# Performance work log

Hardware: AMD Instinct MI355X
Metric: run time of the kernel (lower is better)

Reference implementation:

```python
import jax, jax.numpy as jnp
import numpy as np

H = 512   # GRU hidden
I = 12    # feature dim
Z = 64    # latent dim


def setup_inputs() -> dict:
    key = jax.random.key(0)
    ks = jax.random.split(key, 24)
    B, T = 256, 256
    rn = lambda k, shape, s: (jax.random.normal(k, shape, dtype=jnp.float32) * s)
    sg = 1.0 / np.sqrt(H)
    inp = {
        'x': rn(ks[0], (B, T, I), 1.0),
        'eps': rn(ks[1], (B, Z), 1.0),
        # encoder GRU (torch layout: gates stacked r,z,n)
        'w_ih_e': rn(ks[2], (3 * H, I), sg), 'w_hh_e': rn(ks[3], (3 * H, H), sg),
        'b_ih_e': rn(ks[4], (3 * H,), sg), 'b_hh_e': rn(ks[5], (3 * H,), sg),
        # decoder GRU
        'w_ih_d': rn(ks[6], (3 * H, I), sg), 'w_hh_d': rn(ks[7], (3 * H, H), sg),
        'b_ih_d': rn(ks[8], (3 * H,), sg), 'b_hh_d': rn(ks[9], (3 * H,), sg),
        # linear heads (torch nn.Linear layout: [out, in])
        'fc1_w': rn(ks[10], (256, H), 1 / np.sqrt(H)), 'fc1_b': rn(ks[11], (256,), 0.02),
        'fc11_w': rn(ks[12], (Z, 256), 1 / np.sqrt(256)), 'fc11_b': rn(ks[13], (Z,), 0.02),
        'fc12_w': rn(ks[14], (Z, 256), 1 / np.sqrt(256)), 'fc12_b': rn(ks[15], (Z,), 0.02),
        'fc2_w': rn(ks[16], (256, Z), 1 / np.sqrt(Z)), 'fc2_b': rn(ks[17], (256,), 0.02),
        'fc3_w': rn(ks[18], (H, 256), 1 / np.sqrt(256)), 'fc3_b': rn(ks[19], (H,), 0.02),
        'fc4_w': rn(ks[20], (I, H), 1 / np.sqrt(H)), 'fc4_b': rn(ks[21], (I,), 0.02),
    }
    return inp


def gru_step(x, h, w_ih, w_hh, b_ih, b_hh):
    # torch GRU cell: gates ordered (r, z, n)
    gi = x @ w_ih.T + b_ih            # [B, 3H]
    gh = h @ w_hh.T + b_hh            # [B, 3H]
    i_r, i_z, i_n = jnp.split(gi, 3, axis=-1)
    h_r, h_z, h_n = jnp.split(gh, 3, axis=-1)
    r = jax.nn.sigmoid(i_r + h_r)
    z = jax.nn.sigmoid(i_z + h_z)
    n = jnp.tanh(i_n + r * h_n)
    return (1.0 - z) * n + z * h


def reference(x, eps, w_ih_e, w_hh_e, b_ih_e, b_hh_e, w_ih_d, w_hh_d, b_ih_d, b_hh_d,
              fc1_w, fc1_b, fc11_w, fc11_b, fc12_w, fc12_b, fc2_w, fc2_b,
              fc3_w, fc3_b, fc4_w, fc4_b):
    B, T, _ = x.shape
    lrelu = lambda v: jax.nn.leaky_relu(v, 0.01)

    # ---- encoder GRU over time ----
    h0 = jnp.zeros((B, H), x.dtype)
    def enc(h, xt):
        return gru_step(xt, h, w_ih_e, w_hh_e, b_ih_e, b_hh_e), None
    h_enc, _ = jax.lax.scan(enc, h0, jnp.swapaxes(x, 0, 1))  # final hidden [B,H]

    # ---- latent head ----
    v = lrelu(h_enc)
    v = lrelu(v @ fc1_w.T + fc1_b)
    mu = v @ fc11_w.T + fc11_b
    log_var = v @ fc12_w.T + fc12_b
    std = jnp.exp(0.5 * log_var)
    z_lat = mu + std * eps            # reparameterized rsample

    # ---- decoder init ----
    u = lrelu(z_lat @ fc2_w.T + fc2_b)
    h_dec = u @ fc3_w.T + fc3_b       # [B,H]

    y0 = jnp.zeros((B, I), x.dtype)
    def dec(carry, _):
        y, h = carry
        h = gru_step(y, h, w_ih_d, w_hh_d, b_ih_d, b_hh_d)
        y = h @ fc4_w.T + fc4_b
        return (y, h), y
    _, seq = jax.lax.scan(dec, (y0, h_dec), None, length=T)  # [T,B,I]
    seq = jnp.swapaxes(seq, 0, 1)     # [B,T,I]
    return seq, mu, log_var
```

## Files before the change

kernel.cpp:

```cpp
#include <hip/hip_runtime.h>
#include <hip/hip_bf16.h>

#define DI 12
#define DH 512
#define DT 256
#define DB 256
#define SCOPE __HIP_MEMORY_SCOPE_AGENT

typedef float f32x4 __attribute__((ext_vector_type(4)));
typedef __bf16 bf16x8 __attribute__((ext_vector_type(8)));

__device__ __forceinline__ float sigm(float x) { return 1.f / (1.f + __expf(-x)); }
__device__ __forceinline__ float tanh_f(float x) {
    float xc = fminf(fmaxf(x, -15.f), 15.f);
    float e = __expf(-2.f * xc);
    return (1.f - e) / (1.f + e);
}
__device__ __forceinline__ float lrelu(float x) { return x > 0.f ? x : 0.01f * x; }
__device__ __forceinline__ unsigned short f2bf(float f) {
    return __builtin_bit_cast(unsigned short, (__bf16)f);
}

__device__ __forceinline__ void stage_h(unsigned short* hbuf, const unsigned long long* src2, int tid) {
    unsigned long long tmp[11];
    #pragma unroll
    for (int j = 0; j < 11; ++j) {
        int i = tid + j * 384;
        if (i < 4096) tmp[j] = __hip_atomic_load(src2 + i, __ATOMIC_RELAXED, SCOPE);
    }
    #pragma unroll
    for (int j = 0; j < 11; ++j) {
        int i = tid + j * 384;
        if (i < 4096) {
            int row = i >> 7, dq = i & 127;
            unsigned off = (unsigned)row * 1024u + (((unsigned)(dq * 8)) ^ ((unsigned)((row & 7) << 4)));
            *(unsigned long long*)((char*)hbuf + off) = tmp[j];
        }
    }
}

__device__ __forceinline__ void barrier_wait(const unsigned* fl, int wave, int lane, unsigned gen) {
    if (wave == 0) {
        while (true) {
            unsigned v = __hip_atomic_load(fl + (lane & 31), __ATOMIC_RELAXED, SCOPE);
            if (__all((int)(v >= gen))) break;
            __builtin_amdgcn_s_sleep(1);
        }
        __builtin_amdgcn_fence(__ATOMIC_ACQUIRE, "agent");
    }
}

__device__ __forceinline__ f32x4 mfma_hbuf(const unsigned short* hbuf, const bf16x8* bw,
                                           int arow, int lk) {
    f32x4 acc = {0.f, 0.f, 0.f, 0.f};
    const unsigned rbase = (unsigned)arow * 1024u;
    const unsigned swz = (unsigned)((arow & 7) << 4);
    const char* hb = (const char*)hbuf;
    #pragma unroll
    for (int kk = 0; kk < 16; ++kk) {
        unsigned off = rbase + (((unsigned)(kk * 64 + lk * 16)) ^ swz);
        bf16x8 a = *(const bf16x8*)(hb + off);
        acc = __builtin_amdgcn_mfma_f32_16x16x32_bf16(a, bw[kk], acc, 0, 0, 0);
    }
    return acc;
}

__global__ void init_kernel(unsigned* flE, unsigned* flD) {
    if (blockIdx.x == 0) flE[threadIdx.x] = 0u;
    else flD[threadIdx.x] = 0u;
}

__global__ void prep_kernel(const float* __restrict__ w_ih_d, const float* __restrict__ fc4_w,
                            const float* __restrict__ b_ih_d, const float* __restrict__ fc4_b,
                            unsigned short* __restrict__ W2bf, float* __restrict__ b2,
                            unsigned short* __restrict__ fc4bf)
{
    const int r = blockIdx.x, tid = threadIdx.x;
    if (r < 3 * DH) {
        float wr[DI];
        #pragma unroll
        for (int k = 0; k < DI; ++k) wr[k] = w_ih_d[r * DI + k];
        int c0 = tid * 4;
        #pragma unroll
        for (int q = 0; q < 4; ++q) {
            int c = c0 + q;
            float a = 0.f;
            #pragma unroll
            for (int k = 0; k < DI; ++k) a += wr[k] * fc4_w[k * DH + c];
            W2bf[(size_t)r * DH + c] = f2bf(a);
        }
        if (tid == 0) {
            float a = b_ih_d[r];
            #pragma unroll
            for (int k = 0; k < DI; ++k) a += wr[k] * fc4_b[k];
            b2[r] = a;
        }
    } else {
        int rr = r - 3 * DH;
        int c0 = tid * 4;
        #pragma unroll
        for (int q = 0; q < 4; ++q)
            fc4bf[rr * DH + c0 + q] = (rr < DI) ? f2bf(fc4_w[rr * DH + c0 + q]) : (unsigned short)0;
    }
}

__global__ __launch_bounds__(384, 2)
void enc_kernel(const float* __restrict__ x, const float* __restrict__ w_ih,
                const float* __restrict__ w_hh, const float* __restrict__ b_ih,
                const float* __restrict__ b_hh, unsigned* __restrict__ hpp,
                float* __restrict__ hencF, unsigned* __restrict__ flags)
{
    const int tid = threadIdx.x;
    const int bid = blockIdx.x;
    const int bg = bid & 7;
    const int cb = bid >> 3;
    const int growbase = bg * 32;
    const int ub = cb * 16;
    const int wave = tid >> 6, lane = tid & 63;
    const int rt = wave / 3, g = wave % 3;
    const int lrow = lane & 15, lk = lane >> 4;
    unsigned* flg = flags + bg * 32;

    __shared__ unsigned short hbuf[32 * DH];
    __shared__ float xbuf[32][DI];
    __shared__ float RZ[2][2][16][16];

    const int grow = g * DH + ub + lrow;
    const float bhh_l = b_hh[grow];
    const float bih_l = b_ih[grow];
    float wihr[DI];
    #pragma unroll
    for (int k = 0; k < DI; ++k) wihr[k] = w_ih[grow * DI + k];

    for (int i = tid; i < 32 * DH / 2; i += 384) ((unsigned*)hbuf)[i] = 0u;
    {
        int r = tid / DI, c = tid % DI;
        xbuf[r][c] = x[(size_t)(growbase + r) * (DT * DI) + c];
    }

    bf16x8 bfr[16];
    {
        const float* wr = w_hh + (size_t)grow * DH;
        #pragma unroll
        for (int kk = 0; kk < 16; ++kk) {
            const float* p = wr + kk * 32 + lk * 8;
            bf16x8 v;
            #pragma unroll
            for (int j = 0; j < 8; ++j) v[j] = (__bf16)p[j];
            bfr[kk] = v;
        }
    }
    float hreg[4] = {0.f, 0.f, 0.f, 0.f};
    const int pid = (g != 2) ? ((rt * 2 + g) * 64 + lane) : 0;
    __syncthreads();

    for (int t = 0; t < DT; ++t) {
        const bool lastt = (t == DT - 1);
        f32x4 acc = mfma_hbuf(hbuf, bfr, rt * 16 + lrow, lk);
        float gi[4];
        #pragma unroll
        for (int i = 0; i < 4; ++i) {
            int row = rt * 16 + lk * 4 + i;
            float a2 = bih_l;
            #pragma unroll
            for (int k = 0; k < DI; ++k) a2 += xbuf[row][k] * wihr[k];
            gi[i] = a2;
        }
        float hn[4], gin[4];
        if (g == 0) {
            #pragma unroll
            for (int i = 0; i < 4; ++i)
                RZ[0][rt][lk * 4 + i][lrow] = sigm(acc[i] + bhh_l + gi[i]);
        } else if (g == 1) {
            #pragma unroll
            for (int i = 0; i < 4; ++i)
                RZ[1][rt][lk * 4 + i][lrow] = sigm(acc[i] + bhh_l + gi[i]);
        } else {
            #pragma unroll
            for (int i = 0; i < 4; ++i) { hn[i] = acc[i] + bhh_l; gin[i] = gi[i]; }
        }
        float xr0 = 0.f, xr1 = 0.f;
        if (g != 2 && !lastt) {
            xr0 = x[(size_t)(growbase + pid / 12) * (DT * DI) + (size_t)(t + 1) * DI + pid % 12];
            if (pid < 128) {
                int e = 256 + pid;
                xr1 = x[(size_t)(growbase + e / 12) * (DT * DI) + (size_t)(t + 1) * DI + e % 12];
            }
        }
        __syncthreads();
        if (g == 2) {
            unsigned* dst = hpp + ((t + 1) & 1) * (DB * DH / 2);
            #pragma unroll
            for (int i = 0; i < 4; ++i) {
                int ri = lk * 4 + i;
                int row = rt * 16 + ri;
                float r = RZ[0][rt][ri][lrow];
                float z = RZ[1][rt][ri][lrow];
                float n = tanh_f(gin[i] + r * hn[i]);
                hreg[i] = (1.f - z) * n + z * hreg[i];
                float hp = __shfl_xor(hreg[i], 1);
                if (!lastt) {
                    if (!(lrow & 1)) {
                        unsigned val = (unsigned)f2bf(hreg[i]) | ((unsigned)f2bf(hp) << 16);
                        __hip_atomic_store(dst + (unsigned)(growbase + row) * 256u +
                                           (unsigned)(cb * 8 + (lrow >> 1)),
                                           val, __ATOMIC_RELAXED, SCOPE);
                    }
                } else {
                    hencF[(size_t)(growbase + row) * DH + ub + lrow] = hreg[i];
                }
            }
        }
        if (lastt) break;
        __syncthreads();
        const unsigned gen = (unsigned)(t + 1);
        if (tid == 0) __hip_atomic_store(flg + cb, gen, __ATOMIC_RELAXED, SCOPE);
        barrier_wait(flg, wave, lane, gen);
        __syncthreads();
        stage_h(hbuf, (const unsigned long long*)(hpp + ((t + 1) & 1) * (DB * DH / 2)) +
                      (size_t)growbase * 128, tid);
        if (g != 2) {
            xbuf[pid / 12][pid % 12] = xr0;
            if (pid < 128) { int e = 256 + pid; xbuf[e / 12][e % 12] = xr1; }
        }
        __syncthreads();
    }
}

__global__ void mid_kernel(const float* __restrict__ henc, const float* __restrict__ eps,
                           const float* __restrict__ fc1_w, const float* __restrict__ fc1_b,
                           const float* __restrict__ fc11_w, const float* __restrict__ fc11_b,
                           const float* __restrict__ fc12_w, const float* __restrict__ fc12_b,
                           const float* __restrict__ fc2_w, const float* __restrict__ fc2_b,
                           const float* __restrict__ fc3_w, const float* __restrict__ fc3_b,
                           float* __restrict__ hdecF, unsigned* __restrict__ hppD0,
                           float* __restrict__ out)
{
    const int row = blockIdx.x, tid = threadIdx.x;
    __shared__ float v0[512], v1[256], zb[64], ubuf[256];
    for (int k = tid; k < 512; k += 256) v0[k] = lrelu(henc[(size_t)row * 512 + k]);
    __syncthreads();
    {
        float a = fc1_b[tid];
        const float* w = fc1_w + (size_t)tid * 512;
        for (int k = 0; k < 512; k += 4) {
            float4 wv = *(const float4*)(w + k);
            a += wv.x * v0[k] + wv.y * v0[k + 1] + wv.z * v0[k + 2] + wv.w * v0[k + 3];
        }
        v1[tid] = lrelu(a);
    }
    __syncthreads();
    if (tid < 64) {
        float m = fc11_b[tid], lv = fc12_b[tid];
        const float* w1 = fc11_w + (size_t)tid * 256;
        const float* w2 = fc12_w + (size_t)tid * 256;
        for (int k = 0; k < 256; k += 4) {
            float4 a = *(const float4*)(w1 + k);
            float4 b = *(const float4*)(w2 + k);
            m  += a.x * v1[k] + a.y * v1[k + 1] + a.z * v1[k + 2] + a.w * v1[k + 3];
            lv += b.x * v1[k] + b.y * v1[k + 1] + b.z * v1[k + 2] + b.w * v1[k + 3];
        }
        out[786432 + row * 64 + tid] = m;
        out[802816 + row * 64 + tid] = lv;
        zb[tid] = m + __expf(0.5f * lv) * eps[row * 64 + tid];
    }
    __syncthreads();
    {
        float a = fc2_b[tid];
        const float* w = fc2_w + (size_t)tid * 64;
        for (int k = 0; k < 64; k += 4) {
            float4 wv = *(const float4*)(w + k);
            a += wv.x * zb[k] + wv.y * zb[k + 1] + wv.z * zb[k + 2] + wv.w * zb[k + 3];
        }
        ubuf[tid] = lrelu(a);
    }
    __syncthreads();
    {
        float hv[2];
        #pragma unroll
        for (int q = 0; q < 2; ++q) {
            int j = 2 * tid + q;
            float a = fc3_b[j];
            const float* w = fc3_w + (size_t)j * 256;
            for (int k = 0; k < 256; k += 4) {
                float4 wv = *(const float4*)(w + k);
                a += wv.x * ubuf[k] + wv.y * ubuf[k + 1] + wv.z * ubuf[k + 2] + wv.w * ubuf[k + 3];
            }
            hdecF[(size_t)row * 512 + j] = a;
            hv[q] = a;
        }
        hppD0[row * 256 + tid] = (unsigned)f2bf(hv[0]) | ((unsigned)f2bf(hv[1]) << 16);
    }
}

__global__ __launch_bounds__(384, 2)
void dec_kernel(const float* __restrict__ w_hh, const float* __restrict__ b_ih,
                const float* __restrict__ b_hh, const unsigned short* __restrict__ W2bf,
                const float* __restrict__ b2, const unsigned short* __restrict__ fc4bf,
                const float* __restrict__ fc4_b, const float* __restrict__ hdecF,
                unsigned* __restrict__ hpp, unsigned* __restrict__ flags,
                float* __restrict__ out)
{
    const int tid = threadIdx.x;
    const int bid = blockIdx.x;
    const int bg = bid & 7;
    const int cb = bid >> 3;
    const int growbase = bg * 32;
    const int ub = cb * 16;
    const int wave = tid >> 6, lane = tid & 63;
    const int rt = wave / 3, g = wave % 3;
    const int lrow = lane & 15, lk = lane >> 4;
    unsigned* flg = flags + bg * 32;

    __shared__ unsigned short hbuf[32 * DH];
    __shared__ float RZ[2][2][16][16];

    const int grow = g * DH + ub + lrow;
    const float bhh_l = b_hh[grow];
    const float bih_l = b_ih[grow];
    const float b2_l  = b2[grow];
    const float fb4_l = (lrow < DI) ? fc4_b[lrow] : 0.f;

    bf16x8 bfr[16];
    {
        const float* wr = w_hh + (size_t)grow * DH;
        #pragma unroll
        for (int kk = 0; kk < 16; ++kk) {
            const float* p = wr + kk * 32 + lk * 8;
            bf16x8 v;
            #pragma unroll
            for (int j = 0; j < 8; ++j) v[j] = (__bf16)p[j];
            bfr[kk] = v;
        }
    }
    bf16x8 w2fr[16];
    {
        const unsigned short* wr = W2bf + (size_t)grow * DH;
        #pragma unroll
        for (int kk = 0; kk < 16; ++kk)
            w2fr[kk] = *reinterpret_cast<const bf16x8*>(wr + kk * 32 + lk * 8);
    }
    float hreg[4] = {0.f, 0.f, 0.f, 0.f};
    if (g == 2) {
        #pragma unroll
        for (int i = 0; i < 4; ++i)
            hreg[i] = hdecF[(size_t)(growbase + rt * 16 + lk * 4 + i) * DH + ub + lrow];
    }
    stage_h(hbuf, (const unsigned long long*)hpp + (size_t)growbase * 128, tid);
    __syncthreads();

    const bool ywave = (g == 0) && (cb == 0);
    const unsigned short* fp = fc4bf + (size_t)lrow * DH;

    for (int t = 0; t < DT; ++t) {
        f32x4 acc1 = {0.f, 0.f, 0.f, 0.f};
        f32x4 acc2 = {0.f, 0.f, 0.f, 0.f};
        {
            const int arow = rt * 16 + lrow;
            const unsigned rbase = (unsigned)arow * 1024u;
            const unsigned swz = (unsigned)((arow & 7) << 4);
            const char* hb = (const char*)hbuf;
            if (t == 0) {
                #pragma unroll
                for (int kk = 0; kk < 16; ++kk) {
                    unsigned off = rbase + (((unsigned)(kk * 64 + lk * 16)) ^ swz);
                    bf16x8 a = *(const bf16x8*)(hb + off);
                    acc1 = __builtin_amdgcn_mfma_f32_16x16x32_bf16(a, bfr[kk], acc1, 0, 0, 0);
                }
            } else {
                #pragma unroll
                for (int kk = 0; kk < 16; ++kk) {
                    unsigned off = rbase + (((unsigned)(kk * 64 + lk * 16)) ^ swz);
                    bf16x8 a = *(const bf16x8*)(hb + off);
                    acc1 = __builtin_amdgcn_mfma_f32_16x16x32_bf16(a, bfr[kk], acc1, 0, 0, 0);
                    acc2 = __builtin_amdgcn_mfma_f32_16x16x32_bf16(a, w2fr[kk], acc2, 0, 0, 0);
                }
            }
        }
        if (ywave && t > 0) {
            f32x4 ya = {0.f, 0.f, 0.f, 0.f};
            const int arow = rt * 16 + lrow;
            const unsigned rbase = (unsigned)arow * 1024u;
            const unsigned swz = (unsigned)((arow & 7) << 4);
            const char* hb = (const char*)hbuf;
            #pragma unroll
            for (int kk = 0; kk < 16; ++kk) {
                unsigned off = rbase + (((unsigned)(kk * 64 + lk * 16)) ^ swz);
                bf16x8 a = *(const bf16x8*)(hb + off);
                bf16x8 yb = *reinterpret_cast<const bf16x8*>(fp + kk * 32 + lk * 8);
                ya = __builtin_amdgcn_mfma_f32_16x16x32_bf16(a, yb, ya, 0, 0, 0);
            }
            if (lrow < DI) {
                #pragma unroll
                for (int i = 0; i < 4; ++i)
                    out[(size_t)(growbase + rt * 16 + lk * 4 + i) * (DT * DI) +
                        (size_t)(t - 1) * DI + lrow] = ya[i] + fb4_l;
            }
        }
        const float bsel = (t == 0) ? bih_l : b2_l;
        float hn[4], gin[4];
        if (g == 0) {
            #pragma unroll
            for (int i = 0; i < 4; ++i)
                RZ[0][rt][lk * 4 + i][lrow] = sigm(acc1[i] + bhh_l + acc2[i] + bsel);
        } else if (g == 1) {
            #pragma unroll
            for (int i = 0; i < 4; ++i)
                RZ[1][rt][lk * 4 + i][lrow] = sigm(acc1[i] + bhh_l + acc2[i] + bsel);
        } else {
            #pragma unroll
            for (int i = 0; i < 4; ++i) { hn[i] = acc1[i] + bhh_l; gin[i] = acc2[i] + bsel; }
        }
        __syncthreads();
        if (g == 2) {
            unsigned* dst = hpp + ((t + 1) & 1) * (DB * DH / 2);
            #pragma unroll
            for (int i = 0; i < 4; ++i) {
                int ri = lk * 4 + i;
                int row = rt * 16 + ri;
                float r = RZ[0][rt][ri][lrow];
                float z = RZ[1][rt][ri][lrow];
                float n = tanh_f(gin[i] + r * hn[i]);
                hreg[i] = (1.f - z) * n + z * hreg[i];
                float hp = __shfl_xor(hreg[i], 1);
                if (!(lrow & 1)) {
                    unsigned val = (unsigned)f2bf(hreg[i]) | ((unsigned)f2bf(hp) << 16);
                    __hip_atomic_store(dst + (unsigned)(growbase + row) * 256u +
                                       (unsigned)(cb * 8 + (lrow >> 1)),
                                       val, __ATOMIC_RELAXED, SCOPE);
                }
            }
        }
        __syncthreads();
        const unsigned gen = (unsigned)(t + 1);
        if (tid == 0) __hip_atomic_store(flg + cb, gen, __ATOMIC_RELAXED, SCOPE);
        barrier_wait(flg, wave, lane, gen);
        __syncthreads();
        stage_h(hbuf, (const unsigned long long*)(hpp + ((t + 1) & 1) * (DB * DH / 2)) +
                      (size_t)growbase * 128, tid);
        __syncthreads();
    }
    if (ywave) {
        f32x4 ya = {0.f, 0.f, 0.f, 0.f};
        const int arow = rt * 16 + lrow;
        const unsigned rbase = (unsigned)arow * 1024u;
        const unsigned swz = (unsigned)((arow & 7) << 4);
        const char* hb = (const char*)hbuf;
        #pragma unroll
        for (int kk = 0; kk < 16; ++kk) {
            unsigned off = rbase + (((unsigned)(kk * 64 + lk * 16)) ^ swz);
            bf16x8 a = *(const bf16x8*)(hb + off);
            bf16x8 yb = *reinterpret_cast<const bf16x8*>(fp + kk * 32 + lk * 8);
            ya = __builtin_amdgcn_mfma_f32_16x16x32_bf16(a, yb, ya, 0, 0, 0);
        }
        if (lrow < DI) {
            #pragma unroll
            for (int i = 0; i < 4; ++i)
                out[(size_t)(growbase + rt * 16 + lk * 4 + i) * (DT * DI) +
                    (size_t)(DT - 1) * DI + lrow] = ya[i] + fb4_l;
        }
    }
}

extern "C" void kernel_launch(void* const* d_in, const int* in_sizes, int n_in,
                              void* d_out, int out_size, void* d_ws, size_t ws_size,
                              hipStream_t stream)
{
    const float* x      = (const float*)d_in[0];
    const float* eps    = (const float*)d_in[1];
    const float* w_ih_e = (const float*)d_in[2];
    const float* w_hh_e = (const float*)d_in[3];
    const float* b_ih_e = (const float*)d_in[4];
    const float* b_hh_e = (const float*)d_in[5];
    const float* w_ih_d = (const float*)d_in[6];
    const float* w_hh_d = (const float*)d_in[7];
    const float* b_ih_d = (const float*)d_in[8];
    const float* b_hh_d = (const float*)d_in[9];
    const float* fc1_w  = (const float*)d_in[10];
    const float* fc1_b  = (const float*)d_in[11];
    const float* fc11_w = (const float*)d_in[12];
    const float* fc11_b = (const float*)d_in[13];
    const float* fc12_w = (const float*)d_in[14];
    const float* fc12_b = (const float*)d_in[15];
    const float* fc2_w  = (const float*)d_in[16];
    const float* fc2_b  = (const float*)d_in[17];
    const float* fc3_w  = (const float*)d_in[18];
    const float* fc3_b  = (const float*)d_in[19];
    const float* fc4_w  = (const float*)d_in[20];
    const float* fc4_b  = (const float*)d_in[21];

    char* ws = (char*)d_ws;
    unsigned* hppE        = (unsigned*)(ws + 0);
    unsigned* hppD        = (unsigned*)(ws + 524288);
    float* hencF          = (float*)(ws + 1048576);
    float* hdecF          = (float*)(ws + 1572864);
    unsigned* flagE       = (unsigned*)(ws + 2097152);
    unsigned* flagD       = (unsigned*)(ws + 2101248);
    unsigned short* W2bf  = (unsigned short*)(ws + 2105344);
    float* b2             = (float*)(ws + 3678208);
    unsigned short* fc4bf = (unsigned short*)(ws + 3684352);
    float* out = (float*)d_out;

    init_kernel<<<2, 256, 0, stream>>>(flagE, flagD);
    prep_kernel<<<1552, 128, 0, stream>>>(w_ih_d, fc4_w, b_ih_d, fc4_b, W2bf, b2, fc4bf);
    enc_kernel<<<256, 384, 0, stream>>>(x, w_ih_e, w_hh_e, b_ih_e, b_hh_e, hppE, hencF, flagE);
    mid_kernel<<<256, 256, 0, stream>>>(hencF, eps, fc1_w, fc1_b, fc11_w, fc11_b,
                                        fc12_w, fc12_b, fc2_w, fc2_b, fc3_w, fc3_b,
                                        hdecF, hppD, out);
    dec_kernel<<<256, 384, 0, stream>>>(w_hh_d, b_ih_d, b_hh_d, W2bf, b2, fc4bf, fc4_b,
                                        hdecF, hppD, flagD, out);
}
```

Measured before the change: 3.306 ms.

## Signal per-wave release flags and drop pre-barrier block sync in GRU steps

Each h-producing wave now publishes its own release-ordered flag (64 flags per batch group) as soon as its stores are done, replacing the block-wide __syncthreads plus single-thread relaxed flag store. Polling moves to wave 1, which waits on all 64 flags. In the decoder, the fc4 output MFMA is moved into the else branch so it runs alongside the flag publish and no longer precedes the gate computation. This removes one block barrier per timestep and shortens the critical path between computing h and signalling it. The cost is more flag traffic and a larger polling footprint.

```diff
diff --git a/kernel.cpp b/kernel.cpp
--- a/kernel.cpp
+++ b/kernel.cpp
@@ -39,15 +39,13 @@
     }
 }
 
-__device__ __forceinline__ void barrier_wait(const unsigned* fl, int wave, int lane, unsigned gen) {
-    if (wave == 0) {
-        while (true) {
-            unsigned v = __hip_atomic_load(fl + (lane & 31), __ATOMIC_RELAXED, SCOPE);
-            if (__all((int)(v >= gen))) break;
-            __builtin_amdgcn_s_sleep(1);
-        }
-        __builtin_amdgcn_fence(__ATOMIC_ACQUIRE, "agent");
-    }
+__device__ __forceinline__ void poll64(const unsigned* fl, int lane, unsigned gen) {
+    while (true) {
+        unsigned v = __hip_atomic_load(fl + lane, __ATOMIC_RELAXED, SCOPE);
+        if (__all((int)(v >= gen))) break;
+        __builtin_amdgcn_s_sleep(1);
+    }
+    __builtin_amdgcn_fence(__ATOMIC_ACQUIRE, "agent");
 }
 
 __device__ __forceinline__ f32x4 mfma_hbuf(const unsigned short* hbuf, const bf16x8* bw,
@@ -66,8 +64,9 @@
 }
 
 __global__ void init_kernel(unsigned* flE, unsigned* flD) {
-    if (blockIdx.x == 0) flE[threadIdx.x] = 0u;
-    else flD[threadIdx.x] = 0u;
+    int i = blockIdx.x * 256 + threadIdx.x;
+    if (i < 512) flE[i] = 0u;
+    else flD[i - 512] = 0u;
 }
 
 __global__ void prep_kernel(const float* __restrict__ w_ih_d, const float* __restrict__ fc4_w,
@@ -119,7 +118,7 @@
     const int wave = tid >> 6, lane = tid & 63;
     const int rt = wave / 3, g = wave % 3;
     const int lrow = lane & 15, lk = lane >> 4;
-    unsigned* flg = flags + bg * 32;
+    unsigned* flg = flags + bg * 64;
 
     __shared__ unsigned short hbuf[32 * DH];
     __shared__ float xbuf[32][DI];
@@ -189,33 +188,41 @@
         }
         __syncthreads();
         if (g == 2) {
-            unsigned* dst = hpp + ((t + 1) & 1) * (DB * DH / 2);
-            #pragma unroll
-            for (int i = 0; i < 4; ++i) {
-                int ri = lk * 4 + i;
-                int row = rt * 16 + ri;
-                float r = RZ[0][rt][ri][lrow];
-                float z = RZ[1][rt][ri][lrow];
-                float n = tanh_f(gin[i] + r * hn[i]);
-                hreg[i] = (1.f - z) * n + z * hreg[i];
-                float hp = __shfl_xor(hreg[i], 1);
-                if (!lastt) {
+            if (!lastt) {
+                unsigned* dst = hpp + ((t + 1) & 1) * (DB * DH / 2);
+                #pragma unroll
+                for (int i = 0; i < 4; ++i) {
+                    int ri = lk * 4 + i;
+                    int row = rt * 16 + ri;
+                    float r = RZ[0][rt][ri][lrow];
+                    float z = RZ[1][rt][ri][lrow];
+                    float n = tanh_f(gin[i] + r * hn[i]);
+                    hreg[i] = (1.f - z) * n + z * hreg[i];
+                    float hp = __shfl_xor(hreg[i], 1);
                     if (!(lrow & 1)) {
                         unsigned val = (unsigned)f2bf(hreg[i]) | ((unsigned)f2bf(hp) << 16);
                         __hip_atomic_store(dst + (unsigned)(growbase + row) * 256u +
                                            (unsigned)(cb * 8 + (lrow >> 1)),
                                            val, __ATOMIC_RELAXED, SCOPE);
                     }
-                } else {
+                }
+                if (lane == 0)
+                    __hip_atomic_store(flg + (cb * 2 + rt), (unsigned)(t + 1),
+                                       __ATOMIC_RELEASE, SCOPE);
+            } else {
+                #pragma unroll
+                for (int i = 0; i < 4; ++i) {
+                    int row = rt * 16 + lk * 4 + i;
+                    float r = RZ[0][rt][lk * 4 + i][lrow];
+                    float z = RZ[1][rt][lk * 4 + i][lrow];
+                    float n = tanh_f(gin[i] + r * hn[i]);
+                    hreg[i] = (1.f - z) * n + z * hreg[i];
                     hencF[(size_t)(growbase + row) * DH + ub + lrow] = hreg[i];
                 }
             }
         }
         if (lastt) break;
-        __syncthreads();
-        const unsigned gen = (unsigned)(t + 1);
-        if (tid == 0) __hip_atomic_store(flg + cb, gen, __ATOMIC_RELAXED, SCOPE);
-        barrier_wait(flg, wave, lane, gen);
+        if (wave == 1) poll64(flg, lane, (unsigned)(t + 1));
         __syncthreads();
         stage_h(hbuf, (const unsigned long long*)(hpp + ((t + 1) & 1) * (DB * DH / 2)) +
                       (size_t)growbase * 128, tid);
@@ -310,7 +317,7 @@
     const int wave = tid >> 6, lane = tid & 63;
     const int rt = wave / 3, g = wave % 3;
     const int lrow = lane & 15, lk = lane >> 4;
-    unsigned* flg = flags + bg * 32;
+    unsigned* flg = flags + bg * 64;
 
     __shared__ unsigned short hbuf[32 * DH];
     __shared__ float RZ[2][2][16][16];
@@ -377,26 +384,6 @@
                 }
             }
         }
-        if (ywave && t > 0) {
-            f32x4 ya = {0.f, 0.f, 0.f, 0.f};
-            const int arow = rt * 16 + lrow;
-            const unsigned rbase = (unsigned)arow * 1024u;
-            const unsigned swz = (unsigned)((arow & 7) << 4);
-            const char* hb = (const char*)hbuf;
-            #pragma unroll
-            for (int kk = 0; kk < 16; ++kk) {
-                unsigned off = rbase + (((unsigned)(kk * 64 + lk * 16)) ^ swz);
-                bf16x8 a = *(const bf16x8*)(hb + off);
-                bf16x8 yb = *reinterpret_cast<const bf16x8*>(fp + kk * 32 + lk * 8);
-                ya = __builtin_amdgcn_mfma_f32_16x16x32_bf16(a, yb, ya, 0, 0, 0);
-            }
-            if (lrow < DI) {
-                #pragma unroll
-                for (int i = 0; i < 4; ++i)
-                    out[(size_t)(growbase + rt * 16 + lk * 4 + i) * (DT * DI) +
-                        (size_t)(t - 1) * DI + lrow] = ya[i] + fb4_l;
-            }
-        }
         const float bsel = (t == 0) ? bih_l : b2_l;
         float hn[4], gin[4];
         if (g == 0) {
@@ -430,11 +417,30 @@
                                        val, __ATOMIC_RELAXED, SCOPE);
                 }
             }
-        }
-        __syncthreads();
-        const unsigned gen = (unsigned)(t + 1);
-        if (tid == 0) __hip_atomic_store(flg + cb, gen, __ATOMIC_RELAXED, SCOPE);
-        barrier_wait(flg, wave, lane, gen);
+            if (lane == 0)
+                __hip_atomic_store(flg + (cb * 2 + rt), (unsigned)(t + 1),
+                                   __ATOMIC_RELEASE, SCOPE);
+        } else if (ywave && t > 0) {
+            f32x4 ya = {0.f, 0.f, 0.f, 0.f};
+            const int arow = rt * 16 + lrow;
+            const unsigned rbase = (unsigned)arow * 1024u;
+            const unsigned swz = (unsigned)((arow & 7) << 4);
+            const char* hb = (const char*)hbuf;
+            #pragma unroll
+            for (int kk = 0; kk < 16; ++kk) {
+                unsigned off = rbase + (((unsigned)(kk * 64 + lk * 16)) ^ swz);
+                bf16x8 a = *(const bf16x8*)(hb + off);
+                bf16x8 yb = *reinterpret_cast<const bf16x8*>(fp + kk * 32 + lk * 8);
+                ya = __builtin_amdgcn_mfma_f32_16x16x32_bf16(a, yb, ya, 0, 0, 0);
+            }
+            if (lrow < DI) {
+                #pragma unroll
+                for (int i = 0; i < 4; ++i)
+                    out[(size_t)(growbase + rt * 16 + lk * 4 + i) * (DT * DI) +
+                        (size_t)(t - 1) * DI + lrow] = ya[i] + fb4_l;
+            }
+        }
+        if (wave == 1) poll64(flg, lane, (unsigned)(t + 1));
         __syncthreads();
         stage_h(hbuf, (const unsigned long long*)(hpp + ((t + 1) & 1) * (DB * DH / 2)) +
                       (size_t)growbase * 128, tid);
@@ -495,13 +501,13 @@
     float* hencF          = (float*)(ws + 1048576);
     float* hdecF          = (float*)(ws + 1572864);
     unsigned* flagE       = (unsigned*)(ws + 2097152);
-    unsigned* flagD       = (unsigned*)(ws + 2101248);
-    unsigned short* W2bf  = (unsigned short*)(ws + 2105344);
-    float* b2             = (float*)(ws + 3678208);
-    unsigned short* fc4bf = (unsigned short*)(ws + 3684352);
+    unsigned* flagD       = (unsigned*)(ws + 2099200);
+    unsigned short* W2bf  = (unsigned short*)(ws + 2101248);
+    float* b2             = (float*)(ws + 3674112);
+    unsigned short* fc4bf = (unsigned short*)(ws + 3680256);
     float* out = (float*)d_out;
 
-    init_kernel<<<2, 256, 0, stream>>>(flagE, flagD);
+    init_kernel<<<4, 256, 0, stream>>>(flagE, flagD);
     prep_kernel<<<1552, 128, 0, stream>>>(w_ih_d, fc4_w, b_ih_d, fc4_b, W2bf, b2, fc4bf);
     enc_kernel<<<256, 384, 0, stream>>>(x, w_ih_e, w_hh_e, b_ih_e, b_hh_e, hppE, hencF, flagE);
     mid_kernel<<<256, 256, 0, stream>>>(hencF, eps, fc1_w, fc1_b, fc11_w, fc11_b,
```

Measured after the change: 6.921 ms. +109.3%, slower.
